# Performance work log

Hardware: AMD Instinct MI355X
Metric: run time of the kernel (lower is better)

## Reference

```python
import jax, jax.numpy as jnp
import numpy as np

B, L, D, M = 32, 512, 768, 24  # batch, max_len, bert hidden, mentions per sample
MAX_SPAN = 16


def setup_inputs() -> dict:
    key = jax.random.key(0)
    k1, k2, k3, k4 = jax.random.split(key, 4)
    sequence_output = jax.random.normal(k1, (B, L, D), dtype=jnp.float32)
    head_indexes = jax.random.randint(k2, (B, L), 0, L)
    starts = jax.random.randint(k3, (B, M), 0, L - MAX_SPAN)
    lens = jax.random.randint(k4, (B, M), 1, MAX_SPAN)
    entity_mentions = jnp.stack([starts, starts + lens], axis=-1)  # [B, M, 2], start < end
    return {
        "sequence_output": sequence_output,
        "head_indexes": head_indexes,
        "entity_mentions": entity_mentions,
    }


def reference(sequence_output, head_indexes, entity_mentions):
    b, l, d = sequence_output.shape
    m = entity_mentions.shape[1]

    # per-sample head-token gather: seq[i] = seq[i][head_indexes[i]]
    seq = jnp.take_along_axis(sequence_output, head_indexes[..., None], axis=1)  # [B, L, D]

    # span mean-pool via exclusive prefix sums: mean(seq[s:e]) = (cs[e]-cs[s])/(e-s)
    cs = jnp.concatenate(
        [jnp.zeros((b, 1, d), seq.dtype), jnp.cumsum(seq, axis=1)], axis=1
    )  # [B, L+1, D]
    starts = entity_mentions[..., 0]  # [B, M]
    ends = entity_mentions[..., 1]    # [B, M]
    span_sum = (
        jnp.take_along_axis(cs, ends[..., None], axis=1)
        - jnp.take_along_axis(cs, starts[..., None], axis=1)
    )  # [B, M, D]
    pooled = span_sum / (ends - starts)[..., None].astype(seq.dtype)  # [B, M, D]

    # all ordered pairs i != j (eval path order: i outer, j inner, skip i==j)
    ii, jj = np.meshgrid(np.arange(m), np.arange(m), indexing="ij")
    offdiag = ii != jj
    ii = jnp.asarray(ii[offdiag])  # [P]
    jj = jnp.asarray(jj[offdiag])  # [P]
    p = ii.shape[0]

    obj = pooled[:, ii]  # [B, P, D]
    sub = pooled[:, jj]  # [B, P, D]
    relation_predictions = jnp.concatenate([obj, sub], axis=-1).reshape(b * p, 2 * d)

    batch_idx = jnp.repeat(jnp.arange(b), p)  # [B*P]
    pairs = jnp.stack(
        [
            batch_idx,
            starts[:, ii].reshape(-1),
            ends[:, ii].reshape(-1),
            starts[:, jj].reshape(-1),
            ends[:, jj].reshape(-1),
        ],
        axis=-1,
    )  # [B*P, 5] = [idx, obj_start, obj_end, subj_start, subj_end]
    return relation_predictions, pairs
```

## Files before the change

### kernel.cpp

```cpp
#include <hip/hip_runtime.h>

#define B 32
#define L 512
#define D 768
#define M 24
#define P (M * (M - 1))
#define Q4 (D / 4)

typedef float f32x4 __attribute__((ext_vector_type(4)));

__global__ void fused_kernel(const float* __restrict__ seq,
                             const int*   __restrict__ head,
                             const int*   __restrict__ em,
                             float*       __restrict__ out)
{
    __shared__ f32x4 pool[2][Q4];

    int bm = blockIdx.x;
    int b = bm / M, m = bm - b * M;
    int t  = threadIdx.x;
    int hf = t >= Q4;
    int tq = hf ? t - Q4 : t;

    int s = em[bm * 2 + 0];
    int e = em[bm * 2 + 1];
    int len = e - s;

    const float* seqb  = seq  + (size_t)b * L * D;
    const int*   headb = head + b * L;

    int cnt = (len - hf + 1) >> 1;
    int hidx[8];
    #pragma unroll
    for (int r = 0; r < 8; ++r) {
        int l = s + hf + 2 * r;
        l = (l < e) ? l : s;
        hidx[r] = headb[l];
    }
    f32x4 vv[8];
    #pragma unroll
    for (int r = 0; r < 8; ++r)
        vv[r] = ((const f32x4*)(seqb + (size_t)hidx[r] * D))[tq];
    f32x4 acc = (f32x4)(0.f);
    #pragma unroll
    for (int r = 0; r < 8; ++r)
        acc += (r < cnt) ? vv[r] : (f32x4)(0.f);
    pool[hf][tq] = acc;
    __syncthreads();

    float inv = 1.0f / (float)len;
    f32x4 v = (pool[0][tq] + pool[1][tq]) * inv;

    f32x4* outq = (f32x4*)out;
    size_t rowbase = (size_t)b * P;

    if (!hf) {
        size_t q = (rowbase + (size_t)m * 23) * 384 + tq;
        #pragma unroll
        for (int r = 0; r < 23; ++r) {
            __builtin_nontemporal_store(v, &outq[q]);
            q += 384;
        }
        if (tq < 23) {
            int r = tq;
            int j = (r < m) ? r : r + 1;
            float* o = out + (size_t)B * P * 2 * D
                     + (size_t)(rowbase + (size_t)m * 23 + r) * 5;
            o[0] = (float)b;
            o[1] = (float)s;
            o[2] = (float)e;
            o[3] = (float)em[(b * M + j) * 2 + 0];
            o[4] = (float)em[(b * M + j) * 2 + 1];
        }
    } else {
        #pragma unroll
        for (int i = 0; i < M; ++i) {
            if (i == m) continue;
            int r = (m < i) ? m : m - 1;
            size_t row = rowbase + (size_t)i * 23 + r;
            __builtin_nontemporal_store(v, &outq[row * 384 + Q4 + tq]);
        }
    }
}

extern "C" void kernel_launch(void* const* d_in, const int* in_sizes, int n_in,
                              void* d_out, int out_size, void* d_ws, size_t ws_size,
                              hipStream_t stream) {
    const float* seq  = (const float*)d_in[0];
    const int*   head = (const int*)d_in[1];
    const int*   em   = (const int*)d_in[2];
    float* out = (float*)d_out;

    fused_kernel<<<B * M, 2 * Q4, 0, stream>>>(seq, head, em, out);
}
```

Baseline: 26.72 us.

## Process three mentions per block with prefetch of next span during stores

Each block now handles three mentions in sequence. Both halves of the block redundantly gather all 15 span rows, which removes the shared-memory reduction and the barrier. The gathers for the next mention are issued before the current mention's output stores, so load latency overlaps with the write traffic. In exchange the grid has a third as many blocks, the load count per thread roughly doubles, and 15 live vector registers may raise register pressure.

```diff
diff --git a/kernel.cpp b/kernel.cpp
--- a/kernel.cpp
+++ b/kernel.cpp
@@ -6,79 +6,107 @@
 #define M 24
 #define P (M * (M - 1))
 #define Q4 (D / 4)
+#define MPB 3
+#define NBLK (B * M / MPB)
 
 typedef float f32x4 __attribute__((ext_vector_type(4)));
 
-__global__ void fused_kernel(const float* __restrict__ seq,
-                             const int*   __restrict__ head,
-                             const int*   __restrict__ em,
-                             float*       __restrict__ out)
+__global__ void __launch_bounds__(2 * Q4)
+fused_kernel(const float* __restrict__ seq,
+             const int*   __restrict__ head,
+             const int*   __restrict__ em,
+             float*       __restrict__ out)
 {
-    __shared__ f32x4 pool[2][Q4];
-
-    int bm = blockIdx.x;
-    int b = bm / M, m = bm - b * M;
+    int bk = blockIdx.x;
     int t  = threadIdx.x;
     int hf = t >= Q4;
     int tq = hf ? t - Q4 : t;
 
-    int s = em[bm * 2 + 0];
-    int e = em[bm * 2 + 1];
-    int len = e - s;
+    int bm0 = bk * MPB;
+    int b   = bm0 / M;
+    int m0  = bm0 - b * M;
 
     const float* seqb  = seq  + (size_t)b * L * D;
     const int*   headb = head + b * L;
-
-    int cnt = (len - hf + 1) >> 1;
-    int hidx[8];
-    #pragma unroll
-    for (int r = 0; r < 8; ++r) {
-        int l = s + hf + 2 * r;
-        l = (l < e) ? l : s;
-        hidx[r] = headb[l];
-    }
-    f32x4 vv[8];
-    #pragma unroll
-    for (int r = 0; r < 8; ++r)
-        vv[r] = ((const f32x4*)(seqb + (size_t)hidx[r] * D))[tq];
-    f32x4 acc = (f32x4)(0.f);
-    #pragma unroll
-    for (int r = 0; r < 8; ++r)
-        acc += (r < cnt) ? vv[r] : (f32x4)(0.f);
-    pool[hf][tq] = acc;
-    __syncthreads();
-
-    float inv = 1.0f / (float)len;
-    f32x4 v = (pool[0][tq] + pool[1][tq]) * inv;
+    const int*   emb   = em   + b * M * 2;
 
     f32x4* outq = (f32x4*)out;
+    float* pout = out + (size_t)B * P * 2 * D;
     size_t rowbase = (size_t)b * P;
 
-    if (!hf) {
-        size_t q = (rowbase + (size_t)m * 23) * 384 + tq;
+    int s = emb[2 * m0], e = emb[2 * m0 + 1];
+    int len = e - s;
+    f32x4 acc = (f32x4)(0.f);
+    {
+        int hidx[15];
         #pragma unroll
-        for (int r = 0; r < 23; ++r) {
-            __builtin_nontemporal_store(v, &outq[q]);
-            q += 384;
+        for (int r = 0; r < 15; ++r) {
+            int l = s + r; l = (l < e) ? l : s;
+            hidx[r] = headb[l];
         }
-        if (tq < 23) {
-            int r = tq;
-            int j = (r < m) ? r : r + 1;
-            float* o = out + (size_t)B * P * 2 * D
-                     + (size_t)(rowbase + (size_t)m * 23 + r) * 5;
-            o[0] = (float)b;
-            o[1] = (float)s;
-            o[2] = (float)e;
-            o[3] = (float)em[(b * M + j) * 2 + 0];
-            o[4] = (float)em[(b * M + j) * 2 + 1];
+        f32x4 vv[15];
+        #pragma unroll
+        for (int r = 0; r < 15; ++r)
+            vv[r] = ((const f32x4*)(seqb + (size_t)hidx[r] * D))[tq];
+        #pragma unroll
+        for (int r = 0; r < 15; ++r)
+            acc += (r < len) ? vv[r] : (f32x4)(0.f);
+    }
+
+    #pragma unroll
+    for (int k = 0; k < MPB; ++k) {
+        int m = m0 + k;
+        f32x4 v = acc * (1.0f / (float)len);
+
+        int s_n = 0, e_n = 0, len_n = 0;
+        int hidx[15];
+        f32x4 vv[15];
+        if (k + 1 < MPB) {
+            s_n = emb[2 * (m + 1)]; e_n = emb[2 * (m + 1) + 1];
+            len_n = e_n - s_n;
+            #pragma unroll
+            for (int r = 0; r < 15; ++r) {
+                int l = s_n + r; l = (l < e_n) ? l : s_n;
+                hidx[r] = headb[l];
+            }
+            #pragma unroll
+            for (int r = 0; r < 15; ++r)
+                vv[r] = ((const f32x4*)(seqb + (size_t)hidx[r] * D))[tq];
         }
-    } else {
-        #pragma unroll
-        for (int i = 0; i < M; ++i) {
-            if (i == m) continue;
-            int r = (m < i) ? m : m - 1;
-            size_t row = rowbase + (size_t)i * 23 + r;
-            __builtin_nontemporal_store(v, &outq[row * 384 + Q4 + tq]);
+
+        if (!hf) {
+            size_t q = (rowbase + (size_t)m * 23) * 384 + tq;
+            #pragma unroll
+            for (int r = 0; r < 23; ++r) {
+                __builtin_nontemporal_store(v, &outq[q]);
+                q += 384;
+            }
+            if (tq < 23) {
+                int r = tq;
+                int j = (r < m) ? r : r + 1;
+                float* o = pout + (rowbase + (size_t)m * 23 + r) * 5;
+                o[0] = (float)b;
+                o[1] = (float)s;
+                o[2] = (float)e;
+                o[3] = (float)emb[2 * j];
+                o[4] = (float)emb[2 * j + 1];
+            }
+        } else {
+            #pragma unroll
+            for (int i = 0; i < M; ++i) {
+                if (i == m) continue;
+                int r = (m < i) ? m : m - 1;
+                size_t row = rowbase + (size_t)i * 23 + r;
+                __builtin_nontemporal_store(v, &outq[row * 384 + Q4 + tq]);
+            }
+        }
+
+        if (k + 1 < MPB) {
+            acc = (f32x4)(0.f);
+            #pragma unroll
+            for (int r = 0; r < 15; ++r)
+                acc += (r < len_n) ? vv[r] : (f32x4)(0.f);
+            s = s_n; e = e_n; len = len_n;
         }
     }
 }
@@ -91,5 +119,5 @@
     const int*   em   = (const int*)d_in[2];
     float* out = (float*)d_out;
 
-    fused_kernel<<<B * M, 2 * Q4, 0, stream>>>(seq, head, em, out);
+    fused_kernel<<<NBLK, 2 * Q4, 0, stream>>>(seq, head, em, out);
 }
```

New measurement: 28.76 us. 1.08x slower.

## Split fused kernel into pooling pass and per-pair relation write kernel

Applied to the files above, without the earlier changes.

Replaces the single fused kernel, where each mention block scattered its pooled vector to 23 rows, with two kernels. The first computes the pooled span means into workspace, with one thread per float4 summing up to 15 rows. The second launches one block per output pair row, gathering the two pooled vectors and writing the row contiguously along with its metadata. This gives far more blocks and contiguous writes, at the cost of a second launch and a workspace round trip.

```diff
diff --git a/kernel.cpp b/kernel.cpp
--- a/kernel.cpp
+++ b/kernel.cpp
@@ -9,18 +9,15 @@
 
 typedef float f32x4 __attribute__((ext_vector_type(4)));
 
-__global__ void fused_kernel(const float* __restrict__ seq,
-                             const int*   __restrict__ head,
-                             const int*   __restrict__ em,
-                             float*       __restrict__ out)
+__global__ void __launch_bounds__(Q4)
+pool_kernel(const float* __restrict__ seq,
+            const int*   __restrict__ head,
+            const int*   __restrict__ em,
+            float*       __restrict__ pooled)
 {
-    __shared__ f32x4 pool[2][Q4];
-
     int bm = blockIdx.x;
-    int b = bm / M, m = bm - b * M;
-    int t  = threadIdx.x;
-    int hf = t >= Q4;
-    int tq = hf ? t - Q4 : t;
+    int b = bm / M;
+    int tq = threadIdx.x;
 
     int s = em[bm * 2 + 0];
     int e = em[bm * 2 + 1];
@@ -29,57 +26,51 @@
     const float* seqb  = seq  + (size_t)b * L * D;
     const int*   headb = head + b * L;
 
-    int cnt = (len - hf + 1) >> 1;
-    int hidx[8];
+    int hidx[15];
     #pragma unroll
-    for (int r = 0; r < 8; ++r) {
-        int l = s + hf + 2 * r;
-        l = (l < e) ? l : s;
+    for (int r = 0; r < 15; ++r) {
+        int l = s + r; l = (l < e) ? l : s;
         hidx[r] = headb[l];
     }
-    f32x4 vv[8];
+    f32x4 vv[15];
     #pragma unroll
-    for (int r = 0; r < 8; ++r)
+    for (int r = 0; r < 15; ++r)
         vv[r] = ((const f32x4*)(seqb + (size_t)hidx[r] * D))[tq];
     f32x4 acc = (f32x4)(0.f);
     #pragma unroll
-    for (int r = 0; r < 8; ++r)
-        acc += (r < cnt) ? vv[r] : (f32x4)(0.f);
-    pool[hf][tq] = acc;
-    __syncthreads();
+    for (int r = 0; r < 15; ++r)
+        acc += (r < len) ? vv[r] : (f32x4)(0.f);
+    acc *= 1.0f / (float)len;
 
-    float inv = 1.0f / (float)len;
-    f32x4 v = (pool[0][tq] + pool[1][tq]) * inv;
+    ((f32x4*)pooled)[(size_t)bm * Q4 + tq] = acc;
+}
 
-    f32x4* outq = (f32x4*)out;
-    size_t rowbase = (size_t)b * P;
+__global__ void __launch_bounds__(2 * Q4)
+rel_kernel(const float* __restrict__ pooled,
+           const int*   __restrict__ em,
+           float*       __restrict__ out)
+{
+    int bp = blockIdx.x;
+    int t  = threadIdx.x;
+    int b  = bp / P;
+    int p  = bp - b * P;
+    int i  = p / (M - 1);
+    int r  = p - i * (M - 1);
+    int j  = (r < i) ? r : r + 1;
 
-    if (!hf) {
-        size_t q = (rowbase + (size_t)m * 23) * 384 + tq;
-        #pragma unroll
-        for (int r = 0; r < 23; ++r) {
-            __builtin_nontemporal_store(v, &outq[q]);
-            q += 384;
-        }
-        if (tq < 23) {
-            int r = tq;
-            int j = (r < m) ? r : r + 1;
-            float* o = out + (size_t)B * P * 2 * D
-                     + (size_t)(rowbase + (size_t)m * 23 + r) * 5;
-            o[0] = (float)b;
-            o[1] = (float)s;
-            o[2] = (float)e;
-            o[3] = (float)em[(b * M + j) * 2 + 0];
-            o[4] = (float)em[(b * M + j) * 2 + 1];
-        }
-    } else {
-        #pragma unroll
-        for (int i = 0; i < M; ++i) {
-            if (i == m) continue;
-            int r = (m < i) ? m : m - 1;
-            size_t row = rowbase + (size_t)i * 23 + r;
-            __builtin_nontemporal_store(v, &outq[row * 384 + Q4 + tq]);
-        }
+    int src_m = (t < Q4) ? i : j;
+    int tq    = (t < Q4) ? t : t - Q4;
+    f32x4 v = ((const f32x4*)pooled)[(size_t)(b * M + src_m) * Q4 + tq];
+    __builtin_nontemporal_store(v, &((f32x4*)out)[(size_t)bp * 384 + t]);
+
+    if (t == 0) {
+        const int* emb = em + b * M * 2;
+        float* o = out + (size_t)B * P * 2 * D + (size_t)bp * 5;
+        o[0] = (float)b;
+        o[1] = (float)emb[2 * i];
+        o[2] = (float)emb[2 * i + 1];
+        o[3] = (float)emb[2 * j];
+        o[4] = (float)emb[2 * j + 1];
     }
 }
 
@@ -89,7 +80,9 @@
     const float* seq  = (const float*)d_in[0];
     const int*   head = (const int*)d_in[1];
     const int*   em   = (const int*)d_in[2];
-    float* out = (float*)d_out;
+    float* out    = (float*)d_out;
+    float* pooled = (float*)d_ws;
 
-    fused_kernel<<<B * M, 2 * Q4, 0, stream>>>(seq, head, em, out);
+    pool_kernel<<<B * M, Q4, 0, stream>>>(seq, head, em, pooled);
+    rel_kernel<<<B * P, 2 * Q4, 0, stream>>>(pooled, em, out);
 }
```

After: 30.33 us. 13.5% more time.
